# Kernel tuning notes

Hardware: AMD Instinct MI355X
Metric: run time of the kernel (lower is better)

## Reference

```python
import jax, jax.numpy as jnp
import numpy as np
from jax import lax

ALPHA = 0.5
KERNEL = 25
NUM_P = 16
SEQ_LEN = 1440
PRED_LEN = 720
DWT_LEN = SEQ_LEN // 2 + 2            # 722 (pytorch_wavelets zero-mode, sym3 filt len 6)
FREQ = int(np.ceil(DWT_LEN / 2 * ALPHA) * 2)  # 362

_DEC_LO = np.array([0.035226291882100656, -0.08544127388224149, -0.13501102001039084,
                    0.4598775021193313, 0.8068915093133388, 0.3326705529509569], np.float32)
_DEC_HI = np.array([-0.3326705529509569, 0.8068915093133388, -0.4598775021193313,
                    -0.13501102001039084, 0.08544127388224149, 0.035226291882100656], np.float32)
DEC_LO, DEC_HI = jnp.asarray(_DEC_LO), jnp.asarray(_DEC_HI)
REC_LO, REC_HI = DEC_LO[::-1], DEC_HI[::-1]


def dwt1(x):
    # pytorch_wavelets DWT1DForward(J=1, mode='zero'): zero-pad then stride-2 true conv with dec filters
    B, C, L = x.shape
    out = (L + 5) // 2
    p = 2 * (out - 1) - L + 6
    xp = jnp.pad(x.reshape(B * C, 1, L), ((0, 0), (0, 0), (p // 2, p - p // 2)))
    ker = jnp.stack([DEC_LO[::-1], DEC_HI[::-1]])[:, None, :]   # (2,1,6); xcorr w/ reversed == conv
    y = lax.conv_general_dilated(xp, ker, (2,), 'VALID', dimension_numbers=('NCH', 'OIH', 'NCH'))
    return y[:, 0].reshape(B, C, out), y[:, 1].reshape(B, C, out)


def iwt1(lo, hi):
    # DWT1DInverse mode='zero': conv_transpose stride 2, padding L-2  ->  dilate + conv, pad 1
    B, C, n = lo.shape
    z = jnp.concatenate([lo.reshape(B * C, 1, n), hi.reshape(B * C, 1, n)], axis=1)
    ker = jnp.stack([REC_LO[::-1], REC_HI[::-1]])[None, :, :]   # (O=1, I=2, 6)
    y = lax.conv_general_dilated(z, ker, (1,), [(1, 1)], lhs_dilation=(2,),
                                 dimension_numbers=('NCH', 'OIH', 'NCH'))
    return y[:, 0].reshape(B, C, 2 * n - 4)


def mov_avg(x, k=KERNEL):
    pooled = lax.reduce_window(x, 0.0, lax.add, (1, 1, k), (1, 1, 1), 'VALID') / k
    return jnp.pad(pooled, ((0, 0), (0, 0), (k // 2, k // 2 - (k + 1) % 2)), mode='edge')


def mov_norm(x):
    mean = lax.stop_gradient(mov_avg(x))
    xc = lax.stop_gradient(x - mean)
    std = lax.stop_gradient(mov_avg(jnp.abs(xc))) + 1e-5
    return xc / std, mean, std


def inst_norm(x):
    mean = lax.stop_gradient(jnp.mean(x, -1, keepdims=True))
    xc = x - mean
    var = jnp.mean((xc - jnp.mean(xc, -1, keepdims=True)) ** 2, -1, keepdims=True)
    return xc / jnp.sqrt(var + 1e-5)


def mean_std_mlp(mean, std, mp, sp, mw1, mw2, sw1, sw2, mpred, spred):
    m_all = jnp.mean(mean, -1, keepdims=True)
    s_all = jnp.mean(std, -1, keepdims=True)
    mr = (mean - m_all) @ mp.T
    sr = (std - s_all) @ sp.T
    mr = jax.nn.relu(mr @ mw1.T) @ mw2.T
    sr = jax.nn.relu(sr @ sw1.T) @ sw2.T
    mean_o = mr @ mpred.T + m_all
    std_o = jax.nn.relu(sr @ spred.T + s_all) + 1e-5
    return mean_o, std_o


def forward(x, latent_w, latent_b, acp, dcp):
    xt = jnp.swapaxes(x, -1, 1)                    # (B, C, L)
    ac0, dc0 = dwt1(xt)                            # (B, C, DWT_LEN)
    ac_n = inst_norm(ac0)
    ac, m_ac, s_ac = mov_norm(ac0)
    dc, m_dc, s_dc = mov_norm(dc0)
    m_ac, s_ac = mean_std_mlp(m_ac, s_ac, *acp)    # MLPs[-1]
    m_dc, s_dc = mean_std_mlp(m_dc, s_dc, *dcp)    # MLPs[0]
    dcF = jnp.fft.fft(dc)
    acF = jnp.fft.fft(ac_n)
    idx = jnp.argsort(-jnp.abs(acF), axis=-1)[..., :FREQ]
    amp = ALPHA * jnp.take_along_axis(acF, idx, -1) + (1.0 - ALPHA) * jnp.take_along_axis(dcF, idx, -1)
    B, C, _ = dcF.shape
    bi = jnp.arange(B)[:, None, None]
    ci = jnp.arange(C)[None, :, None]
    dcF = dcF.at[bi, ci, idx].set(amp)
    dc = jnp.real(jnp.fft.ifft(dcF))
    xr = iwt1(ac, dc)                              # (B, C, SEQ_LEN)
    mean = iwt1(m_ac, m_dc)                        # (B, C, PRED_LEN)
    std = iwt1(s_ac, s_dc)
    xr = xr.reshape(B, C, NUM_P, SEQ_LEN // NUM_P)
    emb = xr @ latent_w.T + latent_b               # (B, C, NUM_P, d_model)
    return emb, mean, std


def setup_inputs() -> dict:
    key = jax.random.key(0)
    B, C = 64, 128
    d_model, d_ff = 512, 1024
    s = 0.02
    names_shapes = [
        ('x', (B, SEQ_LEN, C), 1.0),
        ('latent_w', (d_model, SEQ_LEN // NUM_P), s),
    ]
    for pre in ('ac', 'dc'):
        names_shapes += [
            (pre + '_mean_proj', (d_model, DWT_LEN), s),
            (pre + '_std_proj', (d_model, DWT_LEN), s),
            (pre + '_mean_ffn_w1', (d_ff, d_model), s),
            (pre + '_mean_ffn_w2', (d_model, d_ff), s),
            (pre + '_std_ffn_w1', (d_ff, d_model), s),
            (pre + '_std_ffn_w2', (d_model, d_ff), s),
            (pre + '_mean_pred', (PRED_LEN // 2 + 2, d_model), s),
            (pre + '_std_pred', (PRED_LEN // 2 + 2, d_model), s),
        ]
    keys = jax.random.split(key, len(names_shapes))
    inp = {n: jax.random.normal(k, shp, dtype=jnp.float32) * sc
           for (n, shp, sc), k in zip(names_shapes, keys)}
    inp['latent_b'] = jnp.zeros((d_model,), jnp.float32)
    return inp


def reference(x, latent_w, latent_b,
              ac_mean_proj, ac_std_proj, ac_mean_ffn_w1, ac_mean_ffn_w2,
              ac_std_ffn_w1, ac_std_ffn_w2, ac_mean_pred, ac_std_pred,
              dc_mean_proj, dc_std_proj, dc_mean_ffn_w1, dc_mean_ffn_w2,
              dc_std_ffn_w1, dc_std_ffn_w2, dc_mean_pred, dc_std_pred):
    acp = (ac_mean_proj, ac_std_proj, ac_mean_ffn_w1, ac_mean_ffn_w2,
           ac_std_ffn_w1, ac_std_ffn_w2, ac_mean_pred, ac_std_pred)
    dcp = (dc_mean_proj, dc_std_proj, dc_mean_ffn_w1, dc_mean_ffn_w2,
           dc_std_ffn_w1, dc_std_ffn_w2, dc_mean_pred, dc_std_pred)
    return forward(x, latent_w, latent_b, acp, dcp)
```

## Files before the change

### kernel.cpp

```cpp
#include <hip/hip_runtime.h>
#include <cmath>

#define RTOT 8192
#define NDWT 722
#define KP1  736
#define LSEQ 1440
#define NHEAD 362
#define NFREQ 362

typedef __bf16 bf16x8 __attribute__((ext_vector_type(8)));
typedef float f32x4 __attribute__((ext_vector_type(4)));
typedef float f32x2 __attribute__((ext_vector_type(2)));

__device__ __forceinline__ unsigned short f2bf(float f) {
    unsigned u = __float_as_uint(f);
    u += 0x7fffu + ((u >> 16) & 1u);
    return (unsigned short)(u >> 16);
}
__device__ __forceinline__ float bf2f(unsigned short u) {
    return __uint_as_float(((unsigned)u) << 16);
}

__device__ __forceinline__ void cmac(f32x2& s, f32x2 a, f32x2 w) {
    asm("v_pk_fma_f32 %0, %1, %2, %0 op_sel:[0,0,0] op_sel_hi:[0,1,1]\n\t"
        "v_pk_fma_f32 %0, %1, %2, %0 op_sel:[1,1,0] op_sel_hi:[1,0,1] neg_lo:[0,1,0]"
        : "+v"(s) : "v"(a), "v"(w));
}
__device__ __forceinline__ void cmac2(f32x2& s, f32x2 u, f32x2 v, f32x2 w) {
    asm("v_pk_fma_f32 %0, %1, %3, %0 op_sel:[0,0,0] op_sel_hi:[1,0,1]\n\t"
        "v_pk_fma_f32 %0, %2, %3, %0 op_sel:[1,1,0] op_sel_hi:[0,1,1] neg_lo:[0,1,0]"
        : "+v"(s) : "v"(u), "v"(v), "v"(w));
}
__device__ __forceinline__ f32x2 cmul(f32x2 a, f32x2 b) {
    f32x2 r;
    asm("v_pk_mul_f32 %0, %1, %2 op_sel:[0,0] op_sel_hi:[0,1]\n\t"
        "v_pk_fma_f32 %0, %1, %2, %0 op_sel:[1,1,0] op_sel_hi:[1,0,1] neg_lo:[0,1,0]"
        : "=&v"(r) : "v"(a), "v"(b));
    return r;
}

__constant__ float c_lo[6] = {0.035226291882100656f, -0.08544127388224149f, -0.13501102001039084f,
                              0.4598775021193313f, 0.8068915093133388f, 0.3326705529509569f};
__constant__ float c_hi[6] = {-0.3326705529509569f, 0.8068915093133388f, -0.4598775021193313f,
                              -0.13501102001039084f, 0.08544127388224149f, 0.035226291882100656f};

struct CvtDesc { const float* src; unsigned short* dst; int N, K, Np, Kp; };
struct CvtArgs { CvtDesc d[17]; float2* wtab; };
__global__ __launch_bounds__(256) void cvt_all_kernel(CvtArgs a) {
    if (blockIdx.y == 17) {
        int m = blockIdx.x * 256 + threadIdx.x;
        if (m < NDWT) {
            double ang = -2.0 * 3.141592653589793238462643383279502884 * (double)m / (double)NDWT;
            a.wtab[m] = make_float2((float)cos(ang), (float)sin(ang));
        }
        return;
    }
    CvtDesc d = a.d[blockIdx.y];
    int idx = blockIdx.x * 256 + threadIdx.x;
    int tot = d.Np * d.Kp;
    if (idx >= tot) return;
    int r = idx / d.Kp, c = idx - r * d.Kp;
    float v = (r < d.N && c < d.K) ? d.src[(size_t)r * d.K + c] : 0.f;
    d.dst[idx] = f2bf(v);
}

__global__ __launch_bounds__(256) void dwt_kernel(const float* __restrict__ x,
                                                  float* __restrict__ ac0,
                                                  float* __restrict__ dc0) {
    __shared__ float xs[68][129];
    const int b = blockIdx.x;
    const int t0 = blockIdx.y * 32;
    const int tid = threadIdx.x;
    const int lbase = 2 * t0 - 4;
    for (int i = tid; i < 68 * 32; i += 256) {
        int ri = i >> 5;
        int c4 = (i & 31) * 4;
        int l = lbase + ri;
        float4 v = make_float4(0.f, 0.f, 0.f, 0.f);
        if (l >= 0 && l < LSEQ)
            v = *reinterpret_cast<const float4*>(&x[((size_t)b * LSEQ + l) * 128 + c4]);
        xs[ri][c4] = v.x; xs[ri][c4 + 1] = v.y; xs[ri][c4 + 2] = v.z; xs[ri][c4 + 3] = v.w;
    }
    __syncthreads();
    const int tt = tid & 31;
    const int t = t0 + tt;
    const int cw = tid >> 5;
    if (t < NDWT) {
        #pragma unroll 4
        for (int co = 0; co < 16; co++) {
            int c = co * 8 + cw;
            float slo = 0.f, shi = 0.f;
            #pragma unroll
            for (int j = 0; j < 6; j++) {
                float v = xs[2 * tt + 5 - j][c];
                slo += v * c_lo[j];
                shi += v * c_hi[j];
            }
            size_t o = ((size_t)b * 128 + c) * NDWT + t;
            ac0[o] = slo;
            dc0[o] = shi;
        }
    }
}

__device__ __forceinline__ float blockSum256(float v, float* red) {
    #pragma unroll
    for (int o = 32; o > 0; o >>= 1) v += __shfl_down(v, o, 64);
    int lane = threadIdx.x & 63, wid = threadIdx.x >> 6;
    __syncthreads();
    if (lane == 0) red[wid] = v;
    __syncthreads();
    return red[0] + red[1] + red[2] + red[3];
}

template <bool ABS>
__device__ __forceinline__ void pool25(const float* rowv, float* pool, int tid) {
    int i0 = tid * 3;
    if (i0 < 698) {
        float s25 = 0.f;
        #pragma unroll
        for (int j = 0; j < 25; j++) { float v = rowv[i0 + j]; s25 += ABS ? fabsf(v) : v; }
        pool[i0] = s25 * (1.f / 25.f);
        #pragma unroll
        for (int qq = 1; qq < 3; qq++) {
            int i = i0 + qq;
            if (i < 698) {
                float vin = rowv[i + 24], vout = rowv[i - 1];
                s25 += (ABS ? fabsf(vin) : vin) - (ABS ? fabsf(vout) : vout);
                pool[i] = s25 * (1.f / 25.f);
            }
        }
    }
}

__device__ void fft722_dev(f32x2* X, f32x2* T, const f32x2* Wt, const f32x2* W19) {
    const int tid = threadIdx.x;
    if (tid < 190) {
        const int c = tid / 38;
        const int g = tid - c * 38;
        const int p = (g >= 19) ? 1 : 0;
        const int rr = g - 19 * p;
        const int t0 = c * 4;
        const int nt = (c == 4) ? 3 : 4;
        const f32x2* xp = X + 2 * rr + p;
        f32x2 st[4], w[4], s[4];
        f32x2 a0 = xp[0];
        #pragma unroll
        for (int i = 0; i < 4; i++) {
            int ti = t0 + i; if (ti > 18) ti = 0;
            st[i] = W19[ti];
            w[i] = st[i];
            s[i] = a0;
        }
        #pragma unroll
        for (int m = 1; m <= 9; m++) {
            f32x2 a = xp[38 * m];
            f32x2 b = xp[38 * (19 - m)];
            f32x2 u = a + b, v = a - b;
            #pragma unroll
            for (int i = 0; i < 4; i++) {
                cmac2(s[i], u, v, w[i]);
                if (m < 9) w[i] = cmul(w[i], st[i]);
            }
        }
        int m0 = rr * t0;
        f32x2* Tp = T + p * 361 + rr * 19 + t0;
        #pragma unroll
        for (int i = 0; i < 4; i++) {
            if (i < nt) Tp[i] = cmul(s[i], Wt[2 * m0]);
            m0 += rr;
        }
    }
    __syncthreads();
    if (tid < 190) {
        const int c = tid / 38;
        const int g = tid - c * 38;
        const int p = (g >= 19) ? 1 : 0;
        const int t = g - 19 * p;
        const int jj0 = c * 4;
        const int nj = (c == 4) ? 3 : 4;
        const f32x2* Ap = T + p * 361 + t;
        f32x2 st[4], w[4], s[4];
        f32x2 a0 = Ap[0];
        #pragma unroll
        for (int i = 0; i < 4; i++) {
            int jj = jj0 + i; if (jj > 18) jj = 0;
            st[i] = W19[jj];
            w[i] = st[i];
            s[i] = a0;
        }
        #pragma unroll
        for (int m = 1; m <= 9; m++) {
            f32x2 a = Ap[19 * m];
            f32x2 b = Ap[19 * (19 - m)];
            f32x2 u = a + b, v = a - b;
            #pragma unroll
            for (int i = 0; i < 4; i++) {
                cmac2(s[i], u, v, w[i]);
                if (m < 9) w[i] = cmul(w[i], st[i]);
            }
        }
        f32x2* Xp = X + p * 361;
        #pragma unroll
        for (int i = 0; i < 4; i++) {
            int jj = jj0 + i;
            if (i < nj) Xp[t + 19 * jj] = s[i];
        }
    }
    __syncthreads();
    for (int k = tid; k < 361; k += 256) {
        f32x2 e = X[k], o = X[361 + k], w = Wt[k];
        f32x2 tt = {0.f, 0.f};
        cmac(tt, o, w);
        X[k] = e + tt;
        X[361 + k] = e - tt;
    }
    __syncthreads();
}

__global__ __launch_bounds__(256) void stats_fft_kernel(
    const float* __restrict__ ac0in,
    float* __restrict__ dcb,
    float* __restrict__ acp,
    unsigned short* __restrict__ cent,
    float* __restrict__ stat,
    const f32x2* __restrict__ Wtab) {
    __shared__ f32x2 Wt[NDWT];
    __shared__ f32x2 W19s[19];
    __shared__ f32x2 B1[NDWT];
    __shared__ __align__(16) char arena[8704];
    __shared__ unsigned hist[256];
    __shared__ unsigned suf[256];
    __shared__ unsigned sh_digit, sh_rem;
    f32x2* B2   = (f32x2*)arena;
    float* smag = (float*)(arena + 5776);
    float* row  = (float*)arena;
    float* xc   = (float*)(arena + 2888);
    float* pool = (float*)(arena + 5776);
    float* red  = (float*)(arena + 8568);
    const int r = blockIdx.x, tid = threadIdx.x;
    const int lane = tid & 63;
    const size_t base = (size_t)r * NDWT;
    const size_t baseP = (size_t)r * KP1;
    const size_t CS = (size_t)RTOT * KP1;

    for (int i = tid; i < NDWT; i += 256) Wt[i] = Wtab[i];
    if (tid < 19) W19s[tid] = Wtab[38 * tid];

    for (int i = tid; i < NDWT; i += 256) row[i] = ac0in[base + i];
    __syncthreads();
    float s = 0.f;
    for (int i = tid; i < NDWT; i += 256) s += row[i];
    float mean = blockSum256(s, red) * (1.f / 722.f);
    s = 0.f;
    for (int i = tid; i < NDWT; i += 256) s += row[i] - mean;
    float m2 = blockSum256(s, red) * (1.f / 722.f);
    s = 0.f;
    for (int i = tid; i < NDWT; i += 256) { float d = row[i] - mean - m2; s += d * d; }
    float var = blockSum256(s, red) * (1.f / 722.f);
    float inv = 1.f / sqrtf(var + 1e-5f);
    for (int i = tid; i < NDWT; i += 256) B1[i].x = (row[i] - mean) * inv;

    pool25<false>(row, pool, tid);
    __syncthreads();
    float msum = 0.f;
    for (int l = tid; l < NDWT; l += 256) {
        int pi = l - 12; pi = pi < 0 ? 0 : (pi > 697 ? 697 : pi);
        float m = pool[pi];
        msum += m;
        xc[l] = row[l] - m;
    }
    float m_all = blockSum256(msum, red) * (1.f / 722.f);
    __syncthreads();
    pool25<true>(xc, pool, tid);
    __syncthreads();
    float ssum = 0.f;
    for (int l = tid; l < NDWT; l += 256) {
        int pi = l - 12; pi = pi < 0 ? 0 : (pi > 697 ? 697 : pi);
        float sd = pool[pi] + 1e-5f;
        ssum += sd;
        acp[base + l] = xc[l] / sd;
    }
    float s_all = blockSum256(ssum, red) * (1.f / 722.f);
    if (tid == 0) { stat[r] = m_all; stat[RTOT + r] = s_all; }
    for (int l = tid; l < KP1; l += 256) {
        if (l < NDWT) {
            float m = row[l] - xc[l];
            int pi = l - 12; pi = pi < 0 ? 0 : (pi > 697 ? 697 : pi);
            float sd = pool[pi] + 1e-5f;
            cent[baseP + l]      = f2bf(m - m_all);
            cent[CS + baseP + l] = f2bf(sd - s_all);
        } else { cent[baseP + l] = 0; cent[CS + baseP + l] = 0; }
    }
    __syncthreads();

    for (int i = tid; i < NDWT; i += 256) row[i] = dcb[base + i];
    __syncthreads();
    pool25<false>(row, pool, tid);
    __syncthreads();
    float msum2 = 0.f;
    for (int l = tid; l < NDWT; l += 256) {
        int pi = l - 12; pi = pi < 0 ? 0 : (pi > 697 ? 697 : pi);
        float m = pool[pi];
        msum2 += m;
        xc[l] = row[l] - m;
    }
    float m_all2 = blockSum256(msum2, red) * (1.f / 722.f);
    __syncthreads();
    pool25<true>(xc, pool, tid);
    __syncthreads();
    float ssum2 = 0.f;
    for (int l = tid; l < NDWT; l += 256) {
        int pi = l - 12; pi = pi < 0 ? 0 : (pi > 697 ? 697 : pi);
        float sd = pool[pi] + 1e-5f;
        ssum2 += sd;
        B1[l].y = xc[l] / sd;
    }
    float s_all2 = blockSum256(ssum2, red) * (1.f / 722.f);
    if (tid == 0) { stat[2 * RTOT + r] = m_all2; stat[3 * RTOT + r] = s_all2; }
    for (int l = tid; l < KP1; l += 256) {
        if (l < NDWT) {
            float m = row[l] - xc[l];
            int pi = l - 12; pi = pi < 0 ? 0 : (pi > 697 ? 697 : pi);
            float sd = pool[pi] + 1e-5f;
            cent[2 * CS + baseP + l] = f2bf(m - m_all2);
            cent[3 * CS + baseP + l] = f2bf(sd - s_all2);
        } else { cent[2 * CS + baseP + l] = 0; cent[3 * CS + baseP + l] = 0; }
    }
    __syncthreads();

    fft722_dev(B1, B2, Wt, W19s);
    for (int k = tid; k < 362; k += 256) {
        int m = (NDWT - k) % NDWT;
        f32x2 zk = B1[k], zm = B1[m];
        f32x2 ak = {0.5f * (zk.x + zm.x), 0.5f * (zk.y - zm.y)};
        f32x2 dk = {0.5f * (zk.y + zm.y), 0.5f * (zm.x - zk.x)};
        B1[k] = ak; B2[k] = dk;
        smag[k] = ak.x * ak.x + ak.y * ak.y;
        if (m != k) {
            f32x2 am = {0.5f * (zm.x + zk.x), 0.5f * (zm.y - zk.y)};
            f32x2 dm = {0.5f * (zm.y + zk.y), 0.5f * (zk.x - zm.x)};
            B1[m] = am; B2[m] = dm;
            smag[m] = am.x * am.x + am.y * am.y;
        }
    }
    __syncthreads();

    unsigned prefix = 0, rem = NFREQ;
    for (int shift = 24; shift >= 0; shift -= 8) {
        hist[tid] = 0;
        __syncthreads();
        unsigned hm = (shift == 24) ? 0u : (0xFFFFFFFFu << (shift + 8));
        for (int i = tid; i < NDWT; i += 256) {
            unsigned b = __float_as_uint(smag[i]);
            if ((b & hm) == prefix) atomicAdd(&hist[(b >> shift) & 255], 1u);
        }
        __syncthreads();
        if (tid < 64) {
            unsigned h0 = hist[tid * 4 + 0], h1 = hist[tid * 4 + 1];
            unsigned h2 = hist[tid * 4 + 2], h3 = hist[tid * 4 + 3];
            unsigned tot = h0 + h1 + h2 + h3;
            unsigned tinc = tot;
            #pragma unroll
            for (int off = 1; off < 64; off <<= 1) {
                unsigned v = __shfl_down(tinc, off, 64);
                tinc += (lane + off < 64) ? v : 0u;
            }
            unsigned tail = tinc - tot;
            unsigned S3 = tail + h3;
            unsigned S2 = S3 + h2;
            unsigned S1 = S2 + h1;
            unsigned S0 = S1 + h0;
            if (S0 >= rem && S1 < rem) { sh_digit = (unsigned)(tid * 4 + 0); sh_rem = rem - S1; }
            if (S1 >= rem && S2 < rem) { sh_digit = (unsigned)(tid * 4 + 1); sh_rem = rem - S2; }
            if (S2 >= rem && S3 < rem) { sh_digit = (unsigned)(tid * 4 + 2); sh_rem = rem - S3; }
            if (S3 >= rem && tail < rem) { sh_digit = (unsigned)(tid * 4 + 3); sh_rem = rem - tail; }
        }
        __syncthreads();
        prefix |= (sh_digit << shift);
        rem = sh_rem;
    }
    int c0 = tid * 3, cnt = 0;
    #pragma unroll
    for (int j = 0; j < 3; j++) {
        int i = c0 + j;
        if (i < NDWT && __float_as_uint(smag[i]) == prefix) cnt++;
    }
    suf[tid] = (unsigned)cnt;
    __syncthreads();
    if (tid < 64) {
        unsigned p0 = suf[tid * 4 + 0], p1 = suf[tid * 4 + 1];
        unsigned p2 = suf[tid * 4 + 2], p3 = suf[tid * 4 + 3];
        unsigned tot = p0 + p1 + p2 + p3;
        unsigned pinc = tot;
        #pragma unroll
        for (int off = 1; off < 64; off <<= 1) {
            unsigned v = __shfl_up(pinc, off, 64);
            pinc += (lane >= off) ? v : 0u;
        }
        unsigned head = pinc - tot;
        suf[tid * 4 + 0] = head;
        suf[tid * 4 + 1] = head + p0;
        suf[tid * 4 + 2] = head + p0 + p1;
        suf[tid * 4 + 3] = head + p0 + p1 + p2;
    }
    __syncthreads();
    int myexc = (int)suf[tid], o = 0;
    #pragma unroll
    for (int j = 0; j < 3; j++) {
        int i = c0 + j;
        if (i < NDWT) {
            unsigned b = __float_as_uint(smag[i]);
            int f = (b > prefix) ? 1 : 0;
            if (b == prefix) { if ((unsigned)(myexc + o) < rem) f = 1; o++; }
            smag[i] = f ? 1.f : 0.f;
        }
    }
    __syncthreads();

    for (int i = tid; i < NDWT; i += 256) {
        f32x2 d = B2[i];
        if (smag[i] != 0.f) { f32x2 a = B1[i]; d.x = 0.5f * (a.x + d.x); d.y = 0.5f * (a.y + d.y); }
        B1[i] = f32x2{d.x, -d.y};
    }
    __syncthreads();
    fft722_dev(B1, B2, Wt, W19s);
    for (int i = tid; i < NDWT; i += 256) dcb[base + i] = B1[i].x * (1.f / 722.f);
}

__global__ __launch_bounds__(256) void iwt_all_kernel(const unsigned short* __restrict__ heads,
                                                      const float* __restrict__ lo,
                                                      const float* __restrict__ hi,
                                                      float* __restrict__ out_mean,
                                                      float* __restrict__ out_std,
                                                      unsigned short* __restrict__ xrbf) {
    const int r = blockIdx.x;
    const int y = blockIdx.y;
    if (y < 6) {
        const int z = y / 3;
        const int t = (y % 3) * 256 + threadIdx.x;
        if (t >= 720) return;
        const size_t HR = (size_t)RTOT * NHEAD;
        const unsigned short* lp = heads + (size_t)z * HR + (size_t)r * NHEAD;
        const unsigned short* hp = heads + (size_t)(2 + z) * HR + (size_t)r * NHEAD;
        float* out = (z ? out_std : out_mean) + (size_t)r * 720;
        float s = 0.f;
        if (t & 1) {
            int j0 = (t - 1) >> 1;
            #pragma unroll
            for (int i = 0; i < 3; i++) s += bf2f(lp[j0 + i]) * c_lo[2 * i] + bf2f(hp[j0 + i]) * c_hi[2 * i];
        } else {
            int j0 = t >> 1;
            #pragma unroll
            for (int i = 0; i < 3; i++) s += bf2f(lp[j0 + i]) * c_lo[2 * i + 1] + bf2f(hp[j0 + i]) * c_hi[2 * i + 1];
        }
        out[t] = s;
    } else {
        const int yy = y - 6;
        const int t = yy * 256 + threadIdx.x;
        if (yy == 0 && threadIdx.x < 96) {
            int sub = threadIdx.x / 6, c = 90 + threadIdx.x % 6;
            xrbf[((size_t)r * 16 + sub) * 96 + c] = 0;
        }
        if (t >= LSEQ) return;
        const float* lp = lo + (size_t)r * NDWT;
        const float* hp = hi + (size_t)r * NDWT;
        float s = 0.f;
        if (t & 1) {
            int j0 = (t - 1) >> 1;
            #pragma unroll
            for (int i = 0; i < 3; i++) s += lp[j0 + i] * c_lo[2 * i] + hp[j0 + i] * c_hi[2 * i];
        } else {
            int j0 = t >> 1;
            #pragma unroll
            for (int i = 0; i < 3; i++) s += lp[j0 + i] * c_lo[2 * i + 1] + hp[j0 + i] * c_hi[2 * i + 1];
        }
        xrbf[((size_t)r * 16 + t / 90) * 96 + (t % 90)] = f2bf(s);
    }
}

struct ZPtrs { const unsigned short* p[4]; };
template <int EPI>
__global__ __launch_bounds__(256) void mfma_gemm_z(
    const unsigned short* __restrict__ A, int lda, size_t zsA,
    ZPtrs Wz, int ldw,
    void* __restrict__ Cout, int ldc, size_t zsC, int Nc,
    const float* __restrict__ biasBase, const float* __restrict__ cbias,
    int Ksteps) {
    __shared__ unsigned short As[2][128 * 32];
    __shared__ unsigned short Bs[2][128 * 32];
    const int z = blockIdx.z;
    const unsigned short* Az = A + (size_t)z * zsA;
    const unsigned short* W = Wz.p[z];
    const int tid = threadIdx.x;
    const int lane = tid & 63, wid = tid >> 6;
    const int bm = blockIdx.x * 128, bn = blockIdx.y * 128;
    const int wr = (wid >> 1) * 64, wc = (wid & 1) * 64;
    f32x4 acc[4][4] = {};
    const int srow = (lane >> 2);
    const int scol = (lane & 3) * 8;
    const int ch0 = wid * 2, ch1 = wid * 2 + 1;
    const unsigned short* ga0 = Az + (size_t)(bm + ch0 * 16 + srow) * lda + scol;
    const unsigned short* ga1 = Az + (size_t)(bm + ch1 * 16 + srow) * lda + scol;
    const unsigned short* gb0 = W + (size_t)(bn + ch0 * 16 + srow) * ldw + scol;
    const unsigned short* gb1 = W + (size_t)(bn + ch1 * 16 + srow) * ldw + scol;

#define STAGE_GL(buf, ks) do { const int k0_ = (ks) * 32;                                      \
    __builtin_amdgcn_global_load_lds((const __attribute__((address_space(1))) unsigned int*)(ga0 + k0_), \
        (__attribute__((address_space(3))) unsigned int*)(&As[buf][ch0 * 512]), 16, 0, 0);     \
    __builtin_amdgcn_global_load_lds((const __attribute__((address_space(1))) unsigned int*)(gb0 + k0_), \
        (__attribute__((address_space(3))) unsigned int*)(&Bs[buf][ch0 * 512]), 16, 0, 0);     \
    __builtin_amdgcn_global_load_lds((const __attribute__((address_space(1))) unsigned int*)(ga1 + k0_), \
        (__attribute__((address_space(3))) unsigned int*)(&As[buf][ch1 * 512]), 16, 0, 0);     \
    __builtin_amdgcn_global_load_lds((const __attribute__((address_space(1))) unsigned int*)(gb1 + k0_), \
        (__attribute__((address_space(3))) unsigned int*)(&Bs[buf][ch1 * 512]), 16, 0, 0);     \
    } while (0)

    STAGE_GL(0, 0);
    int cur = 0;
    const int kof = (lane >> 4) * 8;
    for (int ks = 0; ks < Ksteps; ks++) {
        if (ks + 1 < Ksteps) {
            STAGE_GL(cur ^ 1, ks + 1);
            asm volatile("s_waitcnt vmcnt(4)" ::: "memory");
        } else {
            asm volatile("s_waitcnt vmcnt(0)" ::: "memory");
        }
        __builtin_amdgcn_s_barrier();
        __builtin_amdgcn_sched_barrier(0);
        bf16x8 af[4], bfr[4];
        #pragma unroll
        for (int m = 0; m < 4; m++)
            af[m] = *reinterpret_cast<const bf16x8*>(&As[cur][(wr + m * 16 + (lane & 15)) * 32 + kof]);
        #pragma unroll
        for (int n = 0; n < 4; n++)
            bfr[n] = *reinterpret_cast<const bf16x8*>(&Bs[cur][(wc + n * 16 + (lane & 15)) * 32 + kof]);
        #pragma unroll
        for (int m = 0; m < 4; m++)
            #pragma unroll
            for (int n = 0; n < 4; n++)
                acc[m][n] = __builtin_amdgcn_mfma_f32_16x16x32_bf16(af[m], bfr[n], acc[m][n], 0, 0, 0);
        __builtin_amdgcn_s_barrier();
        __builtin_amdgcn_sched_barrier(0);
        cur ^= 1;
    }
#undef STAGE_GL

    unsigned short* Cb = (unsigned short*)Cout + (size_t)z * zsC;
    float* Cf = (float*)Cout + (size_t)z * zsC;
    const int crow0 = bm + wr + (lane >> 4) * 4;
    const int ccol0 = bn + wc + (lane & 15);
    #pragma unroll
    for (int m = 0; m < 4; m++) {
        #pragma unroll
        for (int n = 0; n < 4; n++) {
            const int col = ccol0 + n * 16;
            if (col < Nc) {
                #pragma unroll
                for (int q = 0; q < 4; q++) {
                    const int row = crow0 + m * 16 + q;
                    float v = acc[m][n][q];
                    if (EPI == 0) {
                        Cb[(size_t)row * ldc + col] = f2bf(v);
                    } else if (EPI == 1) {
                        Cb[(size_t)row * ldc + col] = f2bf(fmaxf(v, 0.f));
                    } else if (EPI == 4) {
                        Cf[(size_t)row * ldc + col] = v + cbias[col];
                    } else {
                        float ob = biasBase[(size_t)z * RTOT + row];
                        if (z & 1) v = fmaxf(v + ob, 0.f) + 1e-5f;
                        else       v += ob;
                        Cb[(size_t)row * ldc + col] = f2bf(v);
                    }
                }
            }
        }
    }
}

extern "C" void kernel_launch(void* const* d_in, const int* in_sizes, int n_in,
                              void* d_out, int out_size, void* d_ws, size_t ws_size,
                              hipStream_t stream) {
    const float* x = (const float*)d_in[0];
    const float* latent_w = (const float*)d_in[1];
    int p0;
    const float* latent_b;
    if (n_in > 2 && in_sizes[2] == 512) { latent_b = (const float*)d_in[2]; p0 = 3; }
    else                                { latent_b = (const float*)d_in[18]; p0 = 2; }

    char* wp = (char*)d_ws;
    auto alloc = [&](size_t bytes) { char* p = wp; wp += (bytes + 255) & ~(size_t)255; return p; };
    const size_t RN = (size_t)RTOT * NDWT;
    float* ac0b = (float*)alloc(RN * 4);
    float* dcb  = (float*)alloc(RN * 4);
    float* acp  = (float*)alloc(RN * 4);
    float* stat = (float*)alloc(4 * RTOT * 4);
    float2* Wtab = (float2*)alloc(NDWT * 8);
    unsigned short* cent  = (unsigned short*)alloc((size_t)4 * RTOT * KP1 * 2);
    unsigned short* mlpB4 = (unsigned short*)alloc((size_t)4 * RTOT * 512 * 2);
    unsigned short* mlpA4 = (unsigned short*)alloc((size_t)4 * RTOT * 1024 * 2);
    unsigned short* mlpC4 = (unsigned short*)alloc((size_t)4 * RTOT * 512 * 2);
    unsigned short* heads = mlpB4;
    unsigned short* xrbf = mlpC4;
    unsigned short *projW[4], *w1W[4], *w2W[4], *predW[4];
    for (int z = 0; z < 4; z++) {
        projW[z] = (unsigned short*)alloc((size_t)512 * KP1 * 2);
        w1W[z]   = (unsigned short*)alloc((size_t)1024 * 512 * 2);
        w2W[z]   = (unsigned short*)alloc((size_t)512 * 1024 * 2);
        predW[z] = (unsigned short*)alloc((size_t)384 * 512 * 2);
    }
    unsigned short* latwb = (unsigned short*)alloc((size_t)512 * 96 * 2);
    (void)ws_size;

    CvtArgs ca;
    int si = 0;
    for (int z = 0; z < 4; z++) {
        int branch = z >> 1, isStd = z & 1, wb = p0 + branch * 8;
        ca.d[si++] = {(const float*)d_in[wb + isStd],         projW[z], 512, NDWT, 512, KP1};
        ca.d[si++] = {(const float*)d_in[wb + 2 + 2 * isStd], w1W[z], 1024, 512, 1024, 512};
        ca.d[si++] = {(const float*)d_in[wb + 3 + 2 * isStd], w2W[z], 512, 1024, 512, 1024};
        ca.d[si++] = {(const float*)d_in[wb + 6 + isStd],     predW[z], NHEAD, 512, 384, 512};
    }
    ca.d[16] = {latent_w, latwb, 512, 90, 512, 96};
    ca.wtab = Wtab;
    cvt_all_kernel<<<dim3(2048, 18), dim3(256), 0, stream>>>(ca);

    dwt_kernel<<<dim3(64, 23), dim3(256), 0, stream>>>(x, ac0b, dcb);
    stats_fft_kernel<<<dim3(RTOT), dim3(256), 0, stream>>>(
        ac0b, dcb, acp, cent, stat, (const f32x2*)Wtab);

    ZPtrs Zp = {{projW[0], projW[1], projW[2], projW[3]}};
    ZPtrs Z1 = {{w1W[0], w1W[1], w1W[2], w1W[3]}};
    ZPtrs Z2 = {{w2W[0], w2W[1], w2W[2], w2W[3]}};
    ZPtrs Zh = {{predW[0], predW[1], predW[2], predW[3]}};
    mfma_gemm_z<0><<<dim3(64, 4, 4), dim3(256), 0, stream>>>(
        cent, KP1, (size_t)RTOT * KP1, Zp, KP1, mlpB4, 512, (size_t)RTOT * 512, 512, nullptr, nullptr, KP1 / 32);
    mfma_gemm_z<1><<<dim3(64, 8, 4), dim3(256), 0, stream>>>(
        mlpB4, 512, (size_t)RTOT * 512, Z1, 512, mlpA4, 1024, (size_t)RTOT * 1024, 1024, nullptr, nullptr, 16);
    mfma_gemm_z<0><<<dim3(64, 4, 4), dim3(256), 0, stream>>>(
        mlpA4, 1024, (size_t)RTOT * 1024, Z2, 1024, mlpC4, 512, (size_t)RTOT * 512, 512, nullptr, nullptr, 32);
    mfma_gemm_z<5><<<dim3(64, 3, 4), dim3(256), 0, stream>>>(
        mlpC4, 512, (size_t)RTOT * 512, Zh, 512, heads, NHEAD, (size_t)RTOT * NHEAD, NHEAD, stat, nullptr, 16);

    float* out = (float*)d_out;
    float* out_mean = out + (size_t)67108864;
    float* out_std  = out_mean + (size_t)5898240;
    iwt_all_kernel<<<dim3(RTOT, 12), dim3(256), 0, stream>>>(heads, acp, dcb, out_mean, out_std, xrbf);

    ZPtrs Zl = {{latwb, latwb, latwb, latwb}};
    mfma_gemm_z<4><<<dim3(1024, 4, 1), dim3(256), 0, stream>>>(
        xrbf, 96, 0, Zl, 96, out, 512, 0, 512, nullptr, latent_b, 3);
}
```

Before: 507.8 us.

## Fuse input inverse wavelet into stats/FFT kernel and reorder latent GEMM

The inverse wavelet reconstruction of the normalized input is moved into the stats_fft kernel. It reads the AC normalized signal and the filtered DC signal directly from shared memory, so the acp and dcb float buffers no longer round-trip through global memory. xrbf gets its own buffer instead of aliasing mlpC4, which lets the latent GEMM launch right after stats_fft rather than at the end. The remaining heads-only IWT kernel uses a smaller grid. The cost is about 2.9KB more shared memory per block in stats_fft and extra work at its tail.

```diff
diff --git a/kernel.cpp b/kernel.cpp
--- a/kernel.cpp
+++ b/kernel.cpp
@@ -220,14 +220,15 @@
 
 __global__ __launch_bounds__(256) void stats_fft_kernel(
     const float* __restrict__ ac0in,
-    float* __restrict__ dcb,
-    float* __restrict__ acp,
+    const float* __restrict__ dc0in,
     unsigned short* __restrict__ cent,
     float* __restrict__ stat,
+    unsigned short* __restrict__ xrbf,
     const f32x2* __restrict__ Wtab) {
     __shared__ f32x2 Wt[NDWT];
     __shared__ f32x2 W19s[19];
     __shared__ f32x2 B1[NDWT];
+    __shared__ float acpL[NDWT];
     __shared__ __align__(16) char arena[8704];
     __shared__ unsigned hist[256];
     __shared__ unsigned suf[256];
@@ -279,7 +280,7 @@
         int pi = l - 12; pi = pi < 0 ? 0 : (pi > 697 ? 697 : pi);
         float sd = pool[pi] + 1e-5f;
         ssum += sd;
-        acp[base + l] = xc[l] / sd;
+        acpL[l] = xc[l] / sd;
     }
     float s_all = blockSum256(ssum, red) * (1.f / 722.f);
     if (tid == 0) { stat[r] = m_all; stat[RTOT + r] = s_all; }
@@ -294,7 +295,7 @@
     }
     __syncthreads();
 
-    for (int i = tid; i < NDWT; i += 256) row[i] = dcb[base + i];
+    for (int i = tid; i < NDWT; i += 256) row[i] = dc0in[base + i];
     __syncthreads();
     pool25<false>(row, pool, tid);
     __syncthreads();
@@ -425,58 +426,52 @@
     }
     __syncthreads();
     fft722_dev(B1, B2, Wt, W19s);
-    for (int i = tid; i < NDWT; i += 256) dcb[base + i] = B1[i].x * (1.f / 722.f);
-}
-
-__global__ __launch_bounds__(256) void iwt_all_kernel(const unsigned short* __restrict__ heads,
-                                                      const float* __restrict__ lo,
-                                                      const float* __restrict__ hi,
-                                                      float* __restrict__ out_mean,
-                                                      float* __restrict__ out_std,
-                                                      unsigned short* __restrict__ xrbf) {
-    const int r = blockIdx.x;
-    const int y = blockIdx.y;
-    if (y < 6) {
-        const int z = y / 3;
-        const int t = (y % 3) * 256 + threadIdx.x;
-        if (t >= 720) return;
-        const size_t HR = (size_t)RTOT * NHEAD;
-        const unsigned short* lp = heads + (size_t)z * HR + (size_t)r * NHEAD;
-        const unsigned short* hp = heads + (size_t)(2 + z) * HR + (size_t)r * NHEAD;
-        float* out = (z ? out_std : out_mean) + (size_t)r * 720;
-        float s = 0.f;
+
+    const float inv722 = 1.f / 722.f;
+    if (tid < 96) {
+        int sub = tid / 6, c = 90 + tid % 6;
+        xrbf[((size_t)r * 16 + sub) * 96 + c] = 0;
+    }
+    for (int t = tid; t < LSEQ; t += 256) {
+        float sx = 0.f;
         if (t & 1) {
             int j0 = (t - 1) >> 1;
             #pragma unroll
-            for (int i = 0; i < 3; i++) s += bf2f(lp[j0 + i]) * c_lo[2 * i] + bf2f(hp[j0 + i]) * c_hi[2 * i];
+            for (int i = 0; i < 3; i++)
+                sx += acpL[j0 + i] * c_lo[2 * i] + (B1[j0 + i].x * inv722) * c_hi[2 * i];
         } else {
             int j0 = t >> 1;
             #pragma unroll
-            for (int i = 0; i < 3; i++) s += bf2f(lp[j0 + i]) * c_lo[2 * i + 1] + bf2f(hp[j0 + i]) * c_hi[2 * i + 1];
-        }
-        out[t] = s;
+            for (int i = 0; i < 3; i++)
+                sx += acpL[j0 + i] * c_lo[2 * i + 1] + (B1[j0 + i].x * inv722) * c_hi[2 * i + 1];
+        }
+        xrbf[((size_t)r * 16 + t / 90) * 96 + (t % 90)] = f2bf(sx);
+    }
+}
+
+__global__ __launch_bounds__(256) void iwt_heads_kernel(const unsigned short* __restrict__ heads,
+                                                        float* __restrict__ out_mean,
+                                                        float* __restrict__ out_std) {
+    const int r = blockIdx.x;
+    const int y = blockIdx.y;
+    const int z = y / 3;
+    const int t = (y % 3) * 256 + threadIdx.x;
+    if (t >= 720) return;
+    const size_t HR = (size_t)RTOT * NHEAD;
+    const unsigned short* lp = heads + (size_t)z * HR + (size_t)r * NHEAD;
+    const unsigned short* hp = heads + (size_t)(2 + z) * HR + (size_t)r * NHEAD;
+    float* out = (z ? out_std : out_mean) + (size_t)r * 720;
+    float s = 0.f;
+    if (t & 1) {
+        int j0 = (t - 1) >> 1;
+        #pragma unroll
+        for (int i = 0; i < 3; i++) s += bf2f(lp[j0 + i]) * c_lo[2 * i] + bf2f(hp[j0 + i]) * c_hi[2 * i];
     } else {
-        const int yy = y - 6;
-        const int t = yy * 256 + threadIdx.x;
-        if (yy == 0 && threadIdx.x < 96) {
-            int sub = threadIdx.x / 6, c = 90 + threadIdx.x % 6;
-            xrbf[((size_t)r * 16 + sub) * 96 + c] = 0;
-        }
-        if (t >= LSEQ) return;
-        const float* lp = lo + (size_t)r * NDWT;
-        const float* hp = hi + (size_t)r * NDWT;
-        float s = 0.f;
-        if (t & 1) {
-            int j0 = (t - 1) >> 1;
-            #pragma unroll
-            for (int i = 0; i < 3; i++) s += lp[j0 + i] * c_lo[2 * i] + hp[j0 + i] * c_hi[2 * i];
-        } else {
-            int j0 = t >> 1;
-            #pragma unroll
-            for (int i = 0; i < 3; i++) s += lp[j0 + i] * c_lo[2 * i + 1] + hp[j0 + i] * c_hi[2 * i + 1];
-        }
-        xrbf[((size_t)r * 16 + t / 90) * 96 + (t % 90)] = f2bf(s);
-    }
+        int j0 = t >> 1;
+        #pragma unroll
+        for (int i = 0; i < 3; i++) s += bf2f(lp[j0 + i]) * c_lo[2 * i + 1] + bf2f(hp[j0 + i]) * c_hi[2 * i + 1];
+    }
+    out[t] = s;
 }
 
 struct ZPtrs { const unsigned short* p[4]; };
@@ -592,16 +587,15 @@
     auto alloc = [&](size_t bytes) { char* p = wp; wp += (bytes + 255) & ~(size_t)255; return p; };
     const size_t RN = (size_t)RTOT * NDWT;
     float* ac0b = (float*)alloc(RN * 4);
-    float* dcb  = (float*)alloc(RN * 4);
-    float* acp  = (float*)alloc(RN * 4);
+    float* dc0b = (float*)alloc(RN * 4);
     float* stat = (float*)alloc(4 * RTOT * 4);
     float2* Wtab = (float2*)alloc(NDWT * 8);
     unsigned short* cent  = (unsigned short*)alloc((size_t)4 * RTOT * KP1 * 2);
+    unsigned short* xrbf  = (unsigned short*)alloc((size_t)131072 * 96 * 2);
     unsigned short* mlpB4 = (unsigned short*)alloc((size_t)4 * RTOT * 512 * 2);
     unsigned short* mlpA4 = (unsigned short*)alloc((size_t)4 * RTOT * 1024 * 2);
     unsigned short* mlpC4 = (unsigned short*)alloc((size_t)4 * RTOT * 512 * 2);
     unsigned short* heads = mlpB4;
-    unsigned short* xrbf = mlpC4;
     unsigned short *projW[4], *w1W[4], *w2W[4], *predW[4];
     for (int z = 0; z < 4; z++) {
         projW[z] = (unsigned short*)alloc((size_t)512 * KP1 * 2);
@@ -625,9 +619,14 @@
     ca.wtab = Wtab;
     cvt_all_kernel<<<dim3(2048, 18), dim3(256), 0, stream>>>(ca);
 
-    dwt_kernel<<<dim3(64, 23), dim3(256), 0, stream>>>(x, ac0b, dcb);
+    dwt_kernel<<<dim3(64, 23), dim3(256), 0, stream>>>(x, ac0b, dc0b);
     stats_fft_kernel<<<dim3(RTOT), dim3(256), 0, stream>>>(
-        ac0b, dcb, acp, cent, stat, (const f32x2*)Wtab);
+        ac0b, dc0b, cent, stat, xrbf, (const f32x2*)Wtab);
+
+    float* out = (float*)d_out;
+    ZPtrs Zl = {{latwb, latwb, latwb, latwb}};
+    mfma_gemm_z<4><<<dim3(1024, 4, 1), dim3(256), 0, stream>>>(
+        xrbf, 96, 0, Zl, 96, out, 512, 0, 512, nullptr, latent_b, 3);
 
     ZPtrs Zp = {{projW[0], projW[1], projW[2], projW[3]}};
     ZPtrs Z1 = {{w1W[0], w1W[1], w1W[2], w1W[3]}};
@@ -642,12 +641,7 @@
     mfma_gemm_z<5><<<dim3(64, 3, 4), dim3(256), 0, stream>>>(
         mlpC4, 512, (size_t)RTOT * 512, Zh, 512, heads, NHEAD, (size_t)RTOT * NHEAD, NHEAD, stat, nullptr, 16);
 
-    float* out = (float*)d_out;
     float* out_mean = out + (size_t)67108864;
     float* out_std  = out_mean + (size_t)5898240;
-    iwt_all_kernel<<<dim3(RTOT, 12), dim3(256), 0, stream>>>(heads, acp, dcb, out_mean, out_std, xrbf);
-
-    ZPtrs Zl = {{latwb, latwb, latwb, latwb}};
-    mfma_gemm_z<4><<<dim3(1024, 4, 1), dim3(256), 0, stream>>>(
-        xrbf, 96, 0, Zl, 96, out, 512, 0, 512, nullptr, latent_b, 3);
-}
+    iwt_heads_kernel<<<dim3(RTOT, 6), dim3(256), 0, stream>>>(heads, out_mean, out_std);
+}
```

Measured after the change: 509.0 us. About the same (+0.2%).
